# Kernel optimization log

Hardware: AMD Instinct MI355X
Metric: run time of the kernel (lower is better)

## Reference

```python
import jax, jax.numpy as jnp
from jax import lax
import numpy as np

DIM = 768        # d_model (mamba-130m)
D_IN = 1024      # vision encoder feature dim
NQ = 384         # num_queries
NB = 12          # num_blocks
BATCH = 2
LSEQ = 1024      # image tokens
DI = 2 * DIM     # mamba d_inner (expand=2)
DS = 16          # d_state
DC = 4           # d_conv
DTR = 48         # dt_rank = ceil(768/16)
NH = 16          # attention heads
HD = DIM // NH
NM = NB + 2      # mamba instances: fwd-enc, bwd-enc, one per block


def _ln(x, g, b):
    m = jnp.mean(x, -1, keepdims=True)
    v = jnp.mean((x - m) ** 2, -1, keepdims=True)
    return (x - m) * lax.rsqrt(v + 1e-5) * g + b


def _mamba(x, in_w, conv_w, conv_b, xproj_w, dt_w, dt_b, A_log, Dp, out_w):
    # x: (B, L, DIM)
    Bb = x.shape[0]
    xz = x @ in_w.T                      # (B, L, 2*DI)
    xi, z = jnp.split(xz, 2, -1)
    # depthwise causal conv1d over time
    xc = lax.conv_general_dilated(xi.transpose(0, 2, 1), conv_w[:, None, :], (1,),
                                  [(DC - 1, 0)], feature_group_count=DI,
                                  dimension_numbers=('NCH', 'OIH', 'NCH'))
    xc = jax.nn.silu((xc + conv_b[None, :, None]).transpose(0, 2, 1))  # (B, L, DI)
    dbl = xc @ xproj_w.T                 # (B, L, DTR + 2*DS)
    dt, Bm, Cm = jnp.split(dbl, [DTR, DTR + DS], -1)
    dt = jax.nn.softplus(dt @ dt_w.T + dt_b)   # (B, L, DI)
    A = -jnp.exp(A_log)                        # (DI, DS)
    dA = jnp.exp(dt[..., None] * A)            # (B, L, DI, DS)
    dBx = dt[..., None] * Bm[:, :, None, :] * xc[..., None]

    def step(h, inp):
        dA_t, dBx_t, C_t = inp
        h = dA_t * h + dBx_t
        return h, jnp.einsum('bds,bs->bd', h, C_t)

    h0 = jnp.zeros((Bb, DI, DS), x.dtype)
    _, ys = lax.scan(step, h0, (dA.transpose(1, 0, 2, 3), dBx.transpose(1, 0, 2, 3), Cm.transpose(1, 0, 2)))
    y = ys.transpose(1, 0, 2) + Dp * xc
    y = y * jax.nn.silu(z)
    return y @ out_w.T


def _local_allowed(nq, nk):
    # matches Attention.get_local_mask: query i attends to its contiguous key block
    kpq, extra = nk // nq, nk % nq
    i = jnp.arange(nq)
    start = i * kpq + jnp.minimum(i, extra)
    end = start + kpq + (i < extra)
    k = jnp.arange(nk)
    return (k[None, :] >= start[:, None]) & (k[None, :] < end[:, None])


def _mha(q_in, kv, in_w, in_b, out_w, out_b, allowed):
    # nn.MultiheadAttention(dim, 16, batch_first=True) cross-attention
    wq, wk, wv = jnp.split(in_w, 3, 0)
    bq, bk, bv = jnp.split(in_b, 3, 0)
    Bb = q_in.shape[0]
    q = (q_in @ wq.T + bq).reshape(Bb, -1, NH, HD)
    k = (kv @ wk.T + bk).reshape(Bb, -1, NH, HD)
    v = (kv @ wv.T + bv).reshape(Bb, -1, NH, HD)
    s = jnp.einsum('bqhd,bkhd->bhqk', q, k) / np.float32(np.sqrt(HD))
    s = jnp.where(allowed[None, None], s, -jnp.inf)
    a = jax.nn.softmax(s, -1)
    o = jnp.einsum('bhqk,bkhd->bqhd', a, v).reshape(Bb, -1, DIM)
    return o @ out_w.T + out_b


def _model(img_emb, queries, vision_proj_w, vision_proj_b, ln_vision_g, ln_vision_b,
           mamba_in_w, mamba_conv_w, mamba_conv_b, mamba_xproj_w, mamba_dt_w, mamba_dt_b,
           mamba_A_log, mamba_D, mamba_out_w, seq_norm_g, seq_norm_b,
           attn_in_w, attn_in_b, attn_out_w, attn_out_b, cross_w, cross_b):
    mp = lambda i: (mamba_in_w[i], mamba_conv_w[i], mamba_conv_b[i], mamba_xproj_w[i],
                    mamba_dt_w[i], mamba_dt_b[i], mamba_A_log[i], mamba_D[i], mamba_out_w[i])
    feats = _ln(img_emb @ vision_proj_w.T + vision_proj_b, ln_vision_g, ln_vision_b)
    fwd = _mamba(feats, *mp(0))
    bwd = jnp.flip(_mamba(jnp.flip(feats, 1), *mp(1)), 1)
    c = fwd + bwd + feats
    x = jnp.broadcast_to(queries, (img_emb.shape[0], NQ, DIM))
    allowed = _local_allowed(NQ, c.shape[1])
    for l in range(NB):
        x = _ln(x, seq_norm_g[l], seq_norm_b[l])
        x = _mamba(x, *mp(l + 2)) + x
        score = _mha(x, c, attn_in_w[l], attn_in_b[l], attn_out_w[l], attn_out_b[l], allowed)
        x = jnp.concatenate([x, score], -1) @ cross_w[l].T + cross_b[l]
    return x


_model_jit = jax.jit(_model)


def setup_inputs() -> dict:
    key = jax.random.key(0)
    ks = iter(jax.random.split(key, 24))
    rn = lambda shape, s=0.02: jax.random.normal(next(ks), shape, jnp.float32) * s
    A_log = jnp.broadcast_to(jnp.log(jnp.arange(1, DS + 1, dtype=jnp.float32)), (NM, DI, DS))
    return {
        'img_emb': rn((BATCH, LSEQ, D_IN), 1.0),
        'queries': rn((1, NQ, DIM)),
        'vision_proj_w': rn((DIM, D_IN)),
        'vision_proj_b': jnp.zeros((DIM,), jnp.float32),
        'ln_vision_g': jnp.ones((DIM,), jnp.float32),
        'ln_vision_b': jnp.zeros((DIM,), jnp.float32),
        'mamba_in_w': rn((NM, 2 * DI, DIM)),
        'mamba_conv_w': rn((NM, DI, DC), 0.1),
        'mamba_conv_b': jnp.zeros((NM, DI), jnp.float32),
        'mamba_xproj_w': rn((NM, DTR + 2 * DS, DI)),
        'mamba_dt_w': rn((NM, DI, DTR), 0.1),
        'mamba_dt_b': rn((NM, DI), 0.5),
        'mamba_A_log': A_log,
        'mamba_D': jnp.ones((NM, DI), jnp.float32),
        'mamba_out_w': rn((NM, DIM, DI)),
        'seq_norm_g': jnp.ones((NB, DIM), jnp.float32),
        'seq_norm_b': jnp.zeros((NB, DIM), jnp.float32),
        'attn_in_w': rn((NB, 3 * DIM, DIM)),
        'attn_in_b': jnp.zeros((NB, 3 * DIM), jnp.float32),
        'attn_out_w': rn((NB, DIM, DIM)),
        'attn_out_b': jnp.zeros((NB, DIM), jnp.float32),
        'cross_w': rn((NB, DIM, 2 * DIM)),
        'cross_b': jnp.zeros((NB, DIM), jnp.float32),
    }


def reference(img_emb, queries, vision_proj_w, vision_proj_b, ln_vision_g, ln_vision_b,
              mamba_in_w, mamba_conv_w, mamba_conv_b, mamba_xproj_w, mamba_dt_w, mamba_dt_b,
              mamba_A_log, mamba_D, mamba_out_w, seq_norm_g, seq_norm_b,
              attn_in_w, attn_in_b, attn_out_w, attn_out_b, cross_w, cross_b):
    return _model_jit(img_emb, queries, vision_proj_w, vision_proj_b, ln_vision_g, ln_vision_b,
                      mamba_in_w, mamba_conv_w, mamba_conv_b, mamba_xproj_w, mamba_dt_w, mamba_dt_b,
                      mamba_A_log, mamba_D, mamba_out_w, seq_norm_g, seq_norm_b,
                      attn_in_w, attn_in_b, attn_out_w, attn_out_b, cross_w, cross_b)
```

## Files before the change

kernel.cpp:

```cpp
#include <hip/hip_runtime.h>
#include <hip/hip_bf16.h>

#define DIMQ 768
#define D_IN 1024
#define NQ 384
#define NBK 12
#define BATCH 2
#define LSEQ 1024
#define DI 1536
#define DS 16
#define DTR 48
#define NH 16
#define HD 48

typedef __attribute__((ext_vector_type(8))) short short8;
typedef __attribute__((ext_vector_type(4))) float f32x4;

#define GF_BIAS 1
#define GF_SOFTPLUS 2
#define EPI_BIAS 1
#define EPI_ADDT 2

#define LOG2E 1.4426950408889634f

__device__ __forceinline__ unsigned short f2bf(float f) {
    unsigned int u = __builtin_bit_cast(unsigned int, f);
    u = (u + 0x7FFFu + ((u >> 16) & 1u)) >> 16;
    return (unsigned short)u;
}
__device__ __forceinline__ float bf2f(unsigned short h) {
    unsigned int u = ((unsigned int)h) << 16;
    return __builtin_bit_cast(float, u);
}

__device__ __forceinline__ void gload_lds16(const void* g, void* l) {
    __builtin_amdgcn_global_load_lds(
        (const __attribute__((address_space(1))) void*)g,
        (__attribute__((address_space(3))) void*)l, 16, 0, 0);
}

struct WTab {
    const float* src[10];
    long long dstOff[10];
    long long ps[10];
    int cum[10];
    int rows[10], cols[10], dcols[10];
    int n;
    int total;
};

__global__ void wconv_kernel(unsigned short* __restrict__ dst, WTab T)
{
    const int i = blockIdx.x * 256 + threadIdx.x;
    if (i >= T.total) return;
    int sI = 0;
    while (i >= T.cum[sI]) ++sI;
    const int e = i - (sI ? T.cum[sI - 1] : 0);
    const int dcols = T.dcols[sI];
    const int r = e / dcols;
    const int c = e - r * dcols;
    float v = 0.f;
    if (r < T.rows[sI] && c < T.cols[sI]) v = T.src[sI][(long long)r * T.cols[sI] + c];
    const unsigned short h = f2bf(v);
    const unsigned short l = f2bf(v - bf2f(h));
    dst[T.dstOff[sI] + e] = h;
    dst[T.dstOff[sI] + T.ps[sI] + e] = l;
}

struct LTab {
    const float* src[7];
    long long srcStride[7], dstOff[7], ps[7];
    int rows[7], cols[7], dcols[7], cum[7];
};

__global__ __launch_bounds__(256)
void wconv_layers(unsigned short* __restrict__ dst, long long layerStride, int lBase, LTab T)
{
    const int e = blockIdx.x * 256 + threadIdx.x;
    const int l = blockIdx.y + lBase;
    int sI = 0;
    while (e >= T.cum[sI]) ++sI;
    const int eo = e - (sI ? T.cum[sI - 1] : 0);
    const int dc = T.dcols[sI];
    const int r = eo / dc;
    const int c = eo - r * dc;
    float v = 0.f;
    if (r < T.rows[sI] && c < T.cols[sI])
        v = T.src[sI][(long long)l * T.srcStride[sI] + (long long)r * T.cols[sI] + c];
    const unsigned short h = f2bf(v);
    const unsigned short lo2 = f2bf(v - bf2f(h));
    unsigned short* d = dst + (long long)blockIdx.y * layerStride + T.dstOff[sI];
    d[eo] = h;
    d[T.ps[sI] + eo] = lo2;
}

__global__ __launch_bounds__(256, 3)
void gemm_direct(const float* __restrict__ Ag, const unsigned short* __restrict__ Bhl,
                 float* __restrict__ Cg, const float* __restrict__ biasg,
                 int M, int N, int K, int lda, int ldb, int ldc,
                 long long sA, long long sB, long long sC, long long sBias,
                 long long planeB, int flags)
{
    __shared__ __align__(16) unsigned short As[2][2][64][40];
    __shared__ __align__(16) unsigned short Bs[2][2][128][32];

    const int z = blockIdx.z;
    const float* A = Ag + (size_t)z * sA;
    const unsigned short* Bhi = Bhl + (size_t)z * sB;
    const unsigned short* Blo = Bhi + planeB;
    float* C = Cg + (size_t)z * sC;

    const int mBase = blockIdx.x * 64;
    const int nBase = blockIdx.y * 128;
    const int tid = threadIdx.x, lane = tid & 63, wave = tid >> 6;
    const int lm = lane & 15, lq = lane >> 4;
    const int wn = wave * 32;
    const int arow = tid >> 2, aq = tid & 3;
    const int brow = lane >> 2;
    const int bcol = (lane & 3) * 8;

    const int ktiles = (K + 31) >> 5;

    auto issueB = [&](int t, int buf) {
#pragma unroll
        for (int cc = 0; cc < 4; ++cc) {
            const int chunk = wave * 4 + cc;
            const int pl = chunk >> 3;
            const int r16 = chunk & 7;
            const unsigned short* bp = pl ? Blo : Bhi;
            const int n = nBase + r16 * 16 + brow;
            gload_lds16(bp + (size_t)n * ldb + t * 32 + bcol, &Bs[buf][pl][r16 * 16][0]);
        }
    };
    auto loadA = [&](int t, float* v) {
        const int col = t * 32 + aq * 8;
        const float* src = A + (size_t)(mBase + arow) * lda + col;
#pragma unroll
        for (int u = 0; u < 2; ++u) {
            float4 t4 = make_float4(0.f, 0.f, 0.f, 0.f);
            if (col + u * 4 < K) t4 = *(const float4*)(src + u * 4);
            v[u*4+0]=t4.x; v[u*4+1]=t4.y; v[u*4+2]=t4.z; v[u*4+3]=t4.w;
        }
    };
    auto writeA = [&](const float* v, int buf) {
        short8 ph, plv;
#pragma unroll
        for (int j = 0; j < 8; ++j) {
            unsigned short h = f2bf(v[j]);
            ph[j] = (short)h;
            plv[j] = (short)f2bf(v[j] - bf2f(h));
        }
        *(short8*)&As[buf][0][arow][aq * 8] = ph;
        *(short8*)&As[buf][1][arow][aq * 8] = plv;
    };

    float av[8];
    issueB(0, 0);
    loadA(0, av);
    writeA(av, 0);

    f32x4 acc[4][2] = {};
    for (int t = 0; t < ktiles; ++t) {
        const int buf = t & 1;
        __syncthreads();
        const bool more = (t + 1) < ktiles;
        if (more) { issueB(t + 1, buf ^ 1); loadA(t + 1, av); }
        short8 ah[4], al[4], bh[2], bl[2];
#pragma unroll
        for (int i = 0; i < 4; ++i) {
            ah[i] = *(const short8*)&As[buf][0][16*i + lm][lq * 8];
            al[i] = *(const short8*)&As[buf][1][16*i + lm][lq * 8];
        }
#pragma unroll
        for (int j = 0; j < 2; ++j) {
            bh[j] = *(const short8*)&Bs[buf][0][wn + 16*j + lm][lq * 8];
            bl[j] = *(const short8*)&Bs[buf][1][wn + 16*j + lm][lq * 8];
        }
#pragma unroll
        for (int i = 0; i < 4; ++i)
#pragma unroll
            for (int j = 0; j < 2; ++j) {
                acc[i][j] = __builtin_amdgcn_mfma_f32_16x16x32_bf16(ah[i], bh[j], acc[i][j], 0, 0, 0);
                acc[i][j] = __builtin_amdgcn_mfma_f32_16x16x32_bf16(ah[i], bl[j], acc[i][j], 0, 0, 0);
                acc[i][j] = __builtin_amdgcn_mfma_f32_16x16x32_bf16(al[i], bh[j], acc[i][j], 0, 0, 0);
            }
        if (more) writeA(av, buf ^ 1);
    }

#pragma unroll
    for (int i = 0; i < 4; ++i)
#pragma unroll
        for (int j = 0; j < 2; ++j)
#pragma unroll
            for (int r = 0; r < 4; ++r) {
                const int m = mBase + i*16 + lq*4 + r;
                const int n = nBase + wn + j*16 + lm;
                float v = acc[i][j][r];
                if (flags & GF_BIAS)     v += biasg[(size_t)z * sBias + n];
                if (flags & GF_SOFTPLUS) v = (v > 20.f) ? v : log1pf(expf(v));
                C[(size_t)m * ldc + n] = v;
            }
}

__global__ __launch_bounds__(256, 3)
void gemm_splitk(const float* __restrict__ Ag, const unsigned short* __restrict__ Bhl,
                 float* __restrict__ Cp,
                 int M, int kLen, int S, int lda, int ldb, int ldP,
                 long long sA, long long sB, long long planeB)
{
    __shared__ __align__(16) unsigned short As[2][2][64][40];
    __shared__ __align__(16) unsigned short Bs[2][2][128][32];

    const int bz = blockIdx.z;
    const int s = bz % S, z = bz / S;
    const int kOff = s * kLen;
    const float* A = Ag + (size_t)z * sA;
    const unsigned short* Bhi = Bhl + (size_t)z * sB;
    const unsigned short* Blo = Bhi + planeB;

    const int mBase = blockIdx.x * 64;
    const int nBase = blockIdx.y * 128;
    const int tid = threadIdx.x, lane = tid & 63, wave = tid >> 6;
    const int lm = lane & 15, lq = lane >> 4;
    const int wn = wave * 32;
    const int arow = tid >> 2, aq = tid & 3;
    const int brow = lane >> 2;
    const int bcol = (lane & 3) * 8;

    const int ktiles = kLen >> 5;

    auto issueB = [&](int t, int buf) {
#pragma unroll
        for (int cc = 0; cc < 4; ++cc) {
            const int chunk = wave * 4 + cc;
            const int pl = chunk >> 3;
            const int r16 = chunk & 7;
            const unsigned short* bp = pl ? Blo : Bhi;
            const int n = nBase + r16 * 16 + brow;
            gload_lds16(bp + (size_t)n * ldb + kOff + t * 32 + bcol, &Bs[buf][pl][r16 * 16][0]);
        }
    };
    auto loadA = [&](int t, float* v) {
        const float* src = A + (size_t)(mBase + arow) * lda + kOff + t * 32 + aq * 8;
#pragma unroll
        for (int u = 0; u < 2; ++u) {
            const float4 t4 = *(const float4*)(src + u * 4);
            v[u*4+0]=t4.x; v[u*4+1]=t4.y; v[u*4+2]=t4.z; v[u*4+3]=t4.w;
        }
    };
    auto writeA = [&](const float* v, int buf) {
        short8 ph, plv;
#pragma unroll
        for (int j = 0; j < 8; ++j) {
            unsigned short h = f2bf(v[j]);
            ph[j] = (short)h;
            plv[j] = (short)f2bf(v[j] - bf2f(h));
        }
        *(short8*)&As[buf][0][arow][aq * 8] = ph;
        *(short8*)&As[buf][1][arow][aq * 8] = plv;
    };

    float av[8];
    issueB(0, 0);
    loadA(0, av);
    writeA(av, 0);

    f32x4 acc[4][2] = {};
    for (int t = 0; t < ktiles; ++t) {
        const int buf = t & 1;
        __syncthreads();
        const bool more = (t + 1) < ktiles;
        if (more) { issueB(t + 1, buf ^ 1); loadA(t + 1, av); }
        short8 ah[4], al[4], bh[2], bl[2];
#pragma unroll
        for (int i = 0; i < 4; ++i) {
            ah[i] = *(const short8*)&As[buf][0][16*i + lm][lq * 8];
            al[i] = *(const short8*)&As[buf][1][16*i + lm][lq * 8];
        }
#pragma unroll
        for (int j = 0; j < 2; ++j) {
            bh[j] = *(const short8*)&Bs[buf][0][wn + 16*j + lm][lq * 8];
            bl[j] = *(const short8*)&Bs[buf][1][wn + 16*j + lm][lq * 8];
        }
#pragma unroll
        for (int i = 0; i < 4; ++i)
#pragma unroll
            for (int j = 0; j < 2; ++j) {
                acc[i][j] = __builtin_amdgcn_mfma_f32_16x16x32_bf16(ah[i], bh[j], acc[i][j], 0, 0, 0);
                acc[i][j] = __builtin_amdgcn_mfma_f32_16x16x32_bf16(ah[i], bl[j], acc[i][j], 0, 0, 0);
                acc[i][j] = __builtin_amdgcn_mfma_f32_16x16x32_bf16(al[i], bh[j], acc[i][j], 0, 0, 0);
            }
        if (more) writeA(av, buf ^ 1);
    }

    float* Cb = Cp + (size_t)bz * M * ldP;
#pragma unroll
    for (int i = 0; i < 4; ++i)
#pragma unroll
        for (int j = 0; j < 2; ++j)
#pragma unroll
            for (int r = 0; r < 4; ++r) {
                const int m = mBase + i*16 + lq*4 + r;
                const int n = nBase + wn + j*16 + lm;
                Cb[(size_t)m * ldP + n] = acc[i][j][r];
            }
}

__global__ void epi_kernel(const float* __restrict__ Cp, float* __restrict__ outF,
                           const float* __restrict__ bias, const float* __restrict__ addT,
                           int Z, int S, int M, int N, int ldP, int ldOut,
                           long long sOutZ, long long sBiasZ, int ldAdd, int flags)
{
    const int n4 = N >> 2;
    const int idx = blockIdx.x * 256 + threadIdx.x;
    if (idx >= Z * M * n4) return;
    const int c4 = idx % n4;
    const int rem = idx / n4;
    const int m = rem % M;
    const int z = rem / M;
    const int n = c4 * 4;
    const float* base = Cp + ((size_t)z * S * M + m) * ldP + n;
    float4 v = *(const float4*)base;
    for (int s = 1; s < S; ++s) {
        const float4 u = *(const float4*)(base + (size_t)s * M * ldP);
        v.x += u.x; v.y += u.y; v.z += u.z; v.w += u.w;
    }
    if (flags & EPI_BIAS) {
        const float4 b4 = *(const float4*)(bias + (size_t)z * sBiasZ + n);
        v.x += b4.x; v.y += b4.y; v.z += b4.z; v.w += b4.w;
    }
    if (flags & EPI_ADDT) {
        const float4 a4 = *(const float4*)(addT + (size_t)m * ldAdd + n);
        v.x += a4.x; v.y += a4.y; v.z += a4.z; v.w += a4.w;
    }
    *(float4*)(outF + (size_t)z * sOutZ + (size_t)m * ldOut + n) = v;
}

__global__ __launch_bounds__(256)
void epi_ln_kernel(const float* __restrict__ Cp, float* __restrict__ outF,
                   const float* __restrict__ bias,
                   const float* __restrict__ g, const float* __restrict__ b,
                   int S, int M, int ldP)
{
    const int m = blockIdx.x;
    const int tid = threadIdx.x;
    __shared__ float red[8];
    float v[3];
    float s = 0.f, s2 = 0.f;
#pragma unroll
    for (int j = 0; j < 3; ++j) {
        const int n = tid + j * 256;
        const float* pp = Cp + (size_t)m * ldP + n;
        float x = pp[0];
        for (int q = 1; q < S; ++q) x += pp[(size_t)q * M * ldP];
        x += bias[n];
        v[j] = x; s += x; s2 += x * x;
    }
#pragma unroll
    for (int o = 32; o; o >>= 1) { s += __shfl_xor(s, o); s2 += __shfl_xor(s2, o); }
    const int wv = tid >> 6;
    if ((tid & 63) == 0) { red[wv] = s; red[4 + wv] = s2; }
    __syncthreads();
    s  = red[0] + red[1] + red[2] + red[3];
    s2 = red[4] + red[5] + red[6] + red[7];
    const float mean = s * (1.f/768.f);
    const float var  = s2 * (1.f/768.f) - mean * mean;
    const float inv  = rsqrtf(var + 1e-5f);
#pragma unroll
    for (int j = 0; j < 3; ++j) {
        const int n = tid + j * 256;
        outF[(size_t)m * DIMQ + n] = (v[j] - mean) * inv * g[n] + b[n];
    }
}

__global__ void ln_kernel(const float* __restrict__ in, float* __restrict__ out,
                          const float* __restrict__ g, const float* __restrict__ b,
                          int rows, int srcMod)
{
    const int row = blockIdx.x * 4 + (threadIdx.x >> 6);
    const int lane = threadIdx.x & 63;
    if (row >= rows) return;
    const float* p = in + (size_t)(row % srcMod) * DIMQ;
    float v[12], s = 0.f, s2 = 0.f;
#pragma unroll
    for (int j = 0; j < 12; ++j) {
        v[j] = p[j*64 + lane];
        s += v[j];
        s2 += v[j]*v[j];
    }
#pragma unroll
    for (int o = 32; o; o >>= 1) { s += __shfl_xor(s, o); s2 += __shfl_xor(s2, o); }
    const float mean = s * (1.f/768.f);
    const float var  = s2 * (1.f/768.f) - mean*mean;
    const float inv  = rsqrtf(var + 1e-5f);
    float* q = out + (size_t)row * DIMQ;
#pragma unroll
    for (int j = 0; j < 12; ++j) {
        const int c = j*64 + lane;
        q[c] = (v[j] - mean) * inv * g[c] + b[c];
    }
}

__global__ void conv_kernel(const float* __restrict__ xz, float* __restrict__ xc,
                            const float* __restrict__ cw, const float* __restrict__ cb,
                            int Bn, int L, int instShift)
{
    const int idx = blockIdx.x * 256 + threadIdx.x;
    const int total = Bn * L * (DI/4);
    if (idx >= total) return;
    const int d4 = idx % (DI/4);
    const int t  = (idx / (DI/4)) % L;
    const int b  = idx / (L * (DI/4));
    const int inst = b >> instShift;
    const int d = d4 * 4;
    const float* base = xz + (size_t)(b * L) * 3072 + d;
    const float4 w0 = *(const float4*)(cw + (size_t)(inst*DI + d + 0) * 4);
    const float4 w1 = *(const float4*)(cw + (size_t)(inst*DI + d + 1) * 4);
    const float4 w2 = *(const float4*)(cw + (size_t)(inst*DI + d + 2) * 4);
    const float4 w3 = *(const float4*)(cw + (size_t)(inst*DI + d + 3) * 4);
    float4 acc = *(const float4*)(cb + (size_t)inst*DI + d);
    float4 xv[4];
#pragma unroll
    for (int j = 0; j < 4; ++j) {
        const int tt = t - 3 + j;
        xv[j] = (tt >= 0) ? *(const float4*)(base + (size_t)tt * 3072) : make_float4(0,0,0,0);
    }
    acc.x += xv[0].x*w0.x + xv[1].x*w0.y + xv[2].x*w0.z + xv[3].x*w0.w;
    acc.y += xv[0].y*w1.x + xv[1].y*w1.y + xv[2].y*w1.z + xv[3].y*w1.w;
    acc.z += xv[0].z*w2.x + xv[1].z*w2.y + xv[2].z*w2.z + xv[3].z*w2.w;
    acc.w += xv[0].w*w3.x + xv[1].w*w3.y + xv[2].w*w3.z + xv[3].w*w3.w;
    float4 o;
    o.x = acc.x / (1.f + expf(-acc.x));
    o.y = acc.y / (1.f + expf(-acc.y));
    o.z = acc.z / (1.f + expf(-acc.z));
    o.w = acc.w / (1.f + expf(-acc.w));
    *(float4*)(xc + (size_t)(b * L + t) * DI + d) = o;
}

__global__ __launch_bounds__(256)
void scan_p1(const float* __restrict__ dt, const float* __restrict__ dbl,
             const float* __restrict__ xc, const float* __restrict__ A_log,
             float* __restrict__ hend, float* __restrict__ sumdt,
             int L, int CL, int Bn, int instShift)
{
    const int d = blockIdx.x * 256 + threadIdx.x;
    const int b = blockIdx.y;
    const int c = blockIdx.z;
    const int inst = b >> instShift;
    const float* ap = A_log + ((size_t)inst * DI + d) * DS;
    float A2[16];
#pragma unroll
    for (int s = 0; s < 16; ++s) A2[s] = -expf(ap[s]) * LOG2E;
    float h[16] = {};
    float sd = 0.f;
    const int t0 = c * CL;
    const size_t rowbase = (size_t)b * L;
    for (int t = t0; t < t0 + CL; ++t) {
        const size_t row = rowbase + t;
        const float dtv = dt[row * DI + d];
        const float xcv = xc[row * DI + d];
        float Bv[16];
        *(float4*)(Bv + 0)  = *(const float4*)(dbl + row * 80 + 48);
        *(float4*)(Bv + 4)  = *(const float4*)(dbl + row * 80 + 52);
        *(float4*)(Bv + 8)  = *(const float4*)(dbl + row * 80 + 56);
        *(float4*)(Bv + 12) = *(const float4*)(dbl + row * 80 + 60);
        sd += dtv;
        const float bx = dtv * xcv;
#pragma unroll
        for (int s = 0; s < 16; ++s)
            h[s] = exp2f(dtv * A2[s]) * h[s] + bx * Bv[s];
    }
    float* hp = hend + (((size_t)c * Bn + b) * DI + d) * DS;
#pragma unroll
    for (int s = 0; s < 16; s += 4)
        *(float4*)(hp + s) = make_float4(h[s], h[s+1], h[s+2], h[s+3]);
    sumdt[((size_t)c * Bn + b) * DI + d] = sd;
}

__global__ void scan_p2(const float* __restrict__ hend, const float* __restrict__ sumdt,
                        const float* __restrict__ A_log, float* __restrict__ hstart,
                        int NC, int Bn, int instShift)
{
    const int gid = blockIdx.x * 256 + threadIdx.x;
    const int s = gid & 15;
    const int rem = gid >> 4;
    const int d = rem % DI;
    const int b = rem / DI;
    const int inst = b >> instShift;
    const float A2 = -expf(A_log[((size_t)inst * DI + d) * DS + s]) * LOG2E;
    float carry = 0.f;
    for (int c = 0; c < NC; ++c) {
        const size_t off = (((size_t)c * Bn + b) * DI + d) * DS + s;
        hstart[off] = carry;
        carry = exp2f(A2 * sumdt[((size_t)c * Bn + b) * DI + d]) * carry + hend[off];
    }
}

__global__ __launch_bounds__(256)
void scan_p3(const float* __restrict__ dt, const float* __restrict__ dbl,
             const float* __restrict__ xc, const float* __restrict__ xz,
             const float* __restrict__ A_log, const float* __restrict__ Dp,
             const float* __restrict__ hstart, float* __restrict__ y,
             int L, int CL, int Bn, int instShift)
{
    const int d = blockIdx.x * 256 + threadIdx.x;
    const int b = blockIdx.y;
    const int c = blockIdx.z;
    const int inst = b >> instShift;
    const float* ap = A_log + ((size_t)inst * DI + d) * DS;
    float A2[16];
#pragma unroll
    for (int s = 0; s < 16; ++s) A2[s] = -expf(ap[s]) * LOG2E;
    const float Dd = Dp[(size_t)inst * DI + d];
    float h[16];
    const float* hp = hstart + (((size_t)c * Bn + b) * DI + d) * DS;
#pragma unroll
    for (int s = 0; s < 16; s += 4) {
        const float4 t4 = *(const float4*)(hp + s);
        h[s] = t4.x; h[s+1] = t4.y; h[s+2] = t4.z; h[s+3] = t4.w;
    }
    const int t0 = c * CL;
    const size_t rowbase = (size_t)b * L;
    for (int t = t0; t < t0 + CL; ++t) {
        const size_t row = rowbase + t;
        const float dtv = dt[row * DI + d];
        const float xcv = xc[row * DI + d];
        const float zv  = xz[row * 3072 + DI + d];
        float Bv[16], Cv[16];
        *(float4*)(Bv + 0)  = *(const float4*)(dbl + row * 80 + 48);
        *(float4*)(Bv + 4)  = *(const float4*)(dbl + row * 80 + 52);
        *(float4*)(Bv + 8)  = *(const float4*)(dbl + row * 80 + 56);
        *(float4*)(Bv + 12) = *(const float4*)(dbl + row * 80 + 60);
        *(float4*)(Cv + 0)  = *(const float4*)(dbl + row * 80 + 64);
        *(float4*)(Cv + 4)  = *(const float4*)(dbl + row * 80 + 68);
        *(float4*)(Cv + 8)  = *(const float4*)(dbl + row * 80 + 72);
        *(float4*)(Cv + 12) = *(const float4*)(dbl + row * 80 + 76);
        const float bx = dtv * xcv;
#pragma unroll
        for (int s = 0; s < 16; ++s)
            h[s] = exp2f(dtv * A2[s]) * h[s] + bx * Bv[s];
        float p0 = 0.f, p1 = 0.f, p2 = 0.f, p3 = 0.f;
#pragma unroll
        for (int s = 0; s < 4; ++s) {
            p0 += h[s]      * Cv[s];
            p1 += h[s + 4]  * Cv[s + 4];
            p2 += h[s + 8]  * Cv[s + 8];
            p3 += h[s + 12] * Cv[s + 12];
        }
        const float p = (p0 + p1) + (p2 + p3);
        y[row * DI + d] = (p + Dd * xcv) * (zv / (1.f + expf(-zv)));
    }
}

__global__ void attn_kernel(const float* __restrict__ q, const float* __restrict__ kv,
                            float* __restrict__ o)
{
    const int bi = blockIdx.x;
    const int b = bi / NQ, i = bi % NQ;
    const int tid = threadIdx.x;
    const int h = tid >> 2, r = tid & 3;
    int start, len;
    if (i < 256) { start = 3*i; len = 3; } else { start = 2*i + 256; len = 2; }
    const float* qp = q + (size_t)bi * DIMQ + h*48 + r*12;
    float qv[12];
#pragma unroll
    for (int u = 0; u < 12; ++u) qv[u] = qp[u];
    float s[3] = {-1e30f, -1e30f, -1e30f};
    for (int j = 0; j < len; ++j) {
        const float* kp = kv + (size_t)(b*LSEQ + start + j) * 1536 + h*48 + r*12;
        float p = 0.f;
#pragma unroll
        for (int u = 0; u < 12; ++u) p += qv[u] * kp[u];
        p += __shfl_xor(p, 1);
        p += __shfl_xor(p, 2);
        s[j] = p * 0.14433756729740644f;
    }
    const float mx = fmaxf(s[0], fmaxf(s[1], s[2]));
    float e[3];
    e[0] = expf(s[0]-mx); e[1] = expf(s[1]-mx); e[2] = expf(s[2]-mx);
    const float inv = 1.f / (e[0] + e[1] + e[2]);
    float ov[12] = {};
    for (int j = 0; j < len; ++j) {
        const float w = e[j] * inv;
        const float* vp = kv + (size_t)(b*LSEQ + start + j) * 1536 + 768 + h*48 + r*12;
#pragma unroll
        for (int u = 0; u < 12; ++u) ov[u] += w * vp[u];
    }
    float* op = o + (size_t)bi * DIMQ + h*48 + r*12;
#pragma unroll
    for (int u = 0; u < 12; ++u) op[u] = ov[u];
}

__global__ void flip_kernel(float* __restrict__ X2)
{
    const int idx = blockIdx.x * 256 + threadIdx.x;
    if (idx >= 2*1024*192) return;
    const int d4 = idx % 192;
    const int t  = (idx / 192) % 1024;
    const int b  = idx / (192 * 1024);
    const size_t dst = ((size_t)((2+b)*1024 + t)) * DIMQ + d4*4;
    const size_t src = ((size_t)(b*1024 + (1023 - t))) * DIMQ + d4*4;
    *(float4*)(X2 + dst) = *(const float4*)(X2 + src);
}

__global__ void combine_kernel(const float* __restrict__ oe, const float* __restrict__ feats,
                               float* __restrict__ c)
{
    const int idx = blockIdx.x * 256 + threadIdx.x;
    if (idx >= 2*1024*192) return;
    const int d4 = idx % 192;
    const int t  = (idx / 192) % 1024;
    const int b  = idx / (192 * 1024);
    const size_t fw = ((size_t)(b*1024 + t)) * DIMQ + d4*4;
    const size_t bw = ((size_t)((2+b)*1024 + (1023 - t))) * DIMQ + d4*4;
    const float4 a = *(const float4*)(oe + fw);
    const float4 bb = *(const float4*)(oe + bw);
    const float4 f = *(const float4*)(feats + fw);
    float4 o;
    o.x = a.x + bb.x + f.x; o.y = a.y + bb.y + f.y;
    o.z = a.z + bb.z + f.z; o.w = a.w + bb.w + f.w;
    *(float4*)(c + fw) = o;
}

extern "C" void kernel_launch(void* const* d_in, const int* in_sizes, int n_in,
                              void* d_out, int out_size, void* d_ws, size_t ws_size,
                              hipStream_t stream) {
    const float* img_emb  = (const float*)d_in[0];
    const float* queries  = (const float*)d_in[1];
    const float* vis_w    = (const float*)d_in[2];
    const float* vis_b    = (const float*)d_in[3];
    const float* lnv_g    = (const float*)d_in[4];
    const float* lnv_b    = (const float*)d_in[5];
    const float* m_in_w   = (const float*)d_in[6];
    const float* m_conv_w = (const float*)d_in[7];
    const float* m_conv_b = (const float*)d_in[8];
    const float* m_xp_w   = (const float*)d_in[9];
    const float* m_dt_w   = (const float*)d_in[10];
    const float* m_dt_b   = (const float*)d_in[11];
    const float* m_A_log  = (const float*)d_in[12];
    const float* m_D      = (const float*)d_in[13];
    const float* m_out_w  = (const float*)d_in[14];
    const float* sn_g     = (const float*)d_in[15];
    const float* sn_b     = (const float*)d_in[16];
    const float* a_in_w   = (const float*)d_in[17];
    const float* a_in_b   = (const float*)d_in[18];
    const float* a_out_w  = (const float*)d_in[19];
    const float* a_out_b  = (const float*)d_in[20];
    const float* cr_w     = (const float*)d_in[21];
    const float* cr_b     = (const float*)d_in[22];
    float* out = (float*)d_out;

    float* ws = (float*)d_ws;
    auto alloc = [&](size_t n) { float* p = ws; ws += n; return p; };
    float* X2   = alloc((size_t)4096*768);
    float* xzb  = alloc((size_t)4096*3072);
    float* xcb  = alloc((size_t)4096*1536);
    float* dblb = alloc((size_t)4096*80);
    float* dtb  = alloc((size_t)4096*1536);
    float* yb   = alloc((size_t)4096*1536);
    float* oe   = alloc((size_t)4096*768);
    float* cbuf = alloc((size_t)2048*768);
    float* xn   = alloc((size_t)768*768);
    float* x1s  = alloc((size_t)768*1536);
    float* qb   = alloc((size_t)768*768);
    float* ob   = alloc((size_t)768*768);
    float* Cp   = alloc((size_t)2359296);
    unsigned short* wenc = (unsigned short*)alloc((size_t)16908288/2);

    const long long LAYER_USH = 14745600;
    const size_t usedFloats = (size_t)(ws - (float*)d_ws);
    const size_t needFull = (usedFloats + (size_t)12 * (LAYER_USH/2)) * 4;
    const bool bigW = ws_size >= needFull;
    unsigned short* wlayAll = (unsigned short*)ws;

    const size_t kvFloats = (size_t)12 * 2048 * 1536;
    const size_t needKV = needFull + kvFloats * 4;
    const bool kvHoist = bigW && ws_size >= needKV;
    float* kvAll = (float*)(wlayAll + (size_t)12 * LAYER_USH);

    const long long P_VIS = 768LL*1024;
    const long long P_IN  = 3072LL*768;
    const long long P_XP  = 128LL*1536;
    const long long P_DT  = 1536LL*64;
    const long long P_OUT = 768LL*1536;
    const long long P_AIN = 2304LL*768;
    const long long P_AOUT= 768LL*768;
    const long long P_CR  = 768LL*1536;
    const long long off_vis   = 0;
    const long long off_encIn = 2*P_VIS;
    const long long off_encXp = off_encIn + 4*P_IN;
    const long long off_encDt = off_encXp + 4*P_XP;
    const long long off_encOut= off_encDt + 4*P_DT;
    const long long off_in  = 0;
    const long long off_xp  = 2*P_IN;
    const long long off_dt  = off_xp + 2*P_XP;
    const long long off_out = off_dt + 2*P_DT;
    const long long off_aIn = off_out + 2*P_OUT;
    const long long off_aOut= off_aIn + 2*P_AIN;
    const long long off_cr  = off_aOut + 2*P_AOUT;

    auto addSeg = [](WTab& T, const float* src, int rows, int cols, int drows, int dcols,
                     long long dstOff) {
        const int k = T.n;
        T.src[k] = src; T.rows[k] = rows; T.cols[k] = cols; T.dcols[k] = dcols;
        T.ps[k] = (long long)drows * dcols;
        T.dstOff[k] = dstOff;
        T.total += drows * dcols;
        T.cum[k] = T.total;
        T.n = k + 1;
    };

    auto GD = [&](const float* A, const unsigned short* Bhl, long long planeB,
                  float* C, const float* bias,
                  int M, int N, int K, int lda, int ldb, int ldc,
                  long long sA, long long sB, long long sC, long long sBias,
                  int Z, int flags) {
        dim3 grid(M/64, N/128, Z);
        gemm_direct<<<grid, 256, 0, stream>>>(A, Bhl, C, bias, M, N, K, lda, ldb, ldc,
                                              sA, sB, sC, sBias, planeB, flags);
    };
    auto GS = [&](const float* A, const unsigned short* Bhl, long long planeB,
                  int M, int Ntile, int kLen, int S, int lda, int ldb, int ldP,
                  long long sA, long long sB, int Z) {
        dim3 grid(M/64, Ntile/128, Z*S);
        gemm_splitk<<<grid, 256, 0, stream>>>(A, Bhl, Cp, M, kLen, S, lda, ldb, ldP,
                                              sA, sB, planeB);
    };
    auto EPI = [&](float* outF, const float* bias, const float* addT,
                   int Z, int S, int M, int N, int ldP, int ldOut,
                   long long sOutZ, long long sBiasZ, int ldAdd, int flags) {
        const int total = Z * M * (N/4);
        epi_kernel<<<(total+255)/256, 256, 0, stream>>>(Cp, outF, bias, addT, Z, S, M, N,
                                                        ldP, ldOut, sOutZ, sBiasZ, ldAdd, flags);
    };

    {
        WTab T = {}; T.n = 0; T.total = 0;
        addSeg(T, vis_w, 768, 1024, 768, 1024, off_vis);
        addSeg(T, m_in_w,               3072, 768, 3072, 768, off_encIn);
        addSeg(T, m_in_w + 3072*768,    3072, 768, 3072, 768, off_encIn + 2*P_IN);
        addSeg(T, m_xp_w,               80, 1536, 128, 1536, off_encXp);
        addSeg(T, m_xp_w + 80*1536,     80, 1536, 128, 1536, off_encXp + 2*P_XP);
        addSeg(T, m_dt_w,               1536, 48, 1536, 64, off_encDt);
        addSeg(T, m_dt_w + 1536*48,     1536, 48, 1536, 64, off_encDt + 2*P_DT);
        addSeg(T, m_out_w,              768, 1536, 768, 1536, off_encOut);
        addSeg(T, m_out_w + 768*1536,   768, 1536, 768, 1536, off_encOut + 2*P_OUT);
        wconv_kernel<<<(T.total+255)/256, 256, 0, stream>>>(wenc, T);
    }

    LTab LT = {};
    {
        auto seg = [&](int k, const float* src, long long srcStride, int rows, int cols,
                       int drows, int dcols, long long dstOff) {
            LT.src[k] = src; LT.srcStride[k] = srcStride;
            LT.rows[k] = rows; LT.cols[k] = cols; LT.dcols[k] = dcols;
            LT.ps[k] = (long long)drows * dcols; LT.dstOff[k] = dstOff;
            LT.cum[k] = (k ? LT.cum[k-1] : 0) + drows * dcols;
        };
        seg(0, m_in_w  + (size_t)2*3072*768, 3072LL*768, 3072, 768, 3072, 768, off_in);
        seg(1, m_xp_w  + (size_t)2*80*1536,  80LL*1536,  80, 1536, 128, 1536, off_xp);
        seg(2, m_dt_w  + (size_t)2*1536*48,  1536LL*48,  1536, 48, 1536, 64, off_dt);
        seg(3, m_out_w + (size_t)2*768*1536, 768LL*1536, 768, 1536, 768, 1536, off_out);
        seg(4, a_in_w,  2304LL*768, 2304, 768, 2304, 768, off_aIn);
        seg(5, a_out_w, 768LL*768,  768, 768, 768, 768, off_aOut);
        seg(6, cr_w,    768LL*1536, 768, 1536, 768, 1536, off_cr);
    }
    if (bigW)
        wconv_layers<<<dim3(28800, 12), 256, 0, stream>>>(wlayAll, LAYER_USH, 0, LT);

    GD(img_emb, wenc + off_vis, P_VIS, oe, vis_b,
       2048, 768, 1024, 1024, 1024, 768, 0,0,0,0, 1, GF_BIAS);
    ln_kernel<<<512, 256, 0, stream>>>(oe, X2, lnv_g, lnv_b, 2048, 2048);
    flip_kernel<<<(2*1024*192 + 255)/256, 256, 0, stream>>>(X2);

    GD(X2, wenc + off_encIn, P_IN, xzb, nullptr,
       2048, 3072, 768, 768, 768, 3072, 2048LL*768, 2*P_IN, 2048LL*3072, 0, 2, 0);
    conv_kernel<<<(4*1024*384 + 255)/256, 256, 0, stream>>>(xzb, xcb, m_conv_w, m_conv_b, 4, 1024, 1);
    GS(xcb, wenc + off_encXp, P_XP, 2048, 128, 384, 4, 1536, 1536, 128,
       2048LL*1536, 2*P_XP, 2);
    EPI(dblb, nullptr, nullptr, 2, 4, 2048, 80, 128, 80, 2048LL*80, 0, 0, 0);
    GD(dblb, wenc + off_encDt, P_DT, dtb, m_dt_b,
       2048, 1536, 48, 80, 64, 1536, 2048LL*80, 2*P_DT, 2048LL*1536, 1536, 2,
       GF_BIAS | GF_SOFTPLUS);
    {
        const int NC = 16, CL = 64;
        float* hend   = oe;
        float* hstart = oe + (size_t)NC*4*DI*DS;
        float* sumdt  = cbuf;
        scan_p1<<<dim3(6, 4, NC), 256, 0, stream>>>(dtb, dblb, xcb, m_A_log, hend, sumdt, 1024, CL, 4, 1);
        scan_p2<<<(4*DI*DS)/256, 256, 0, stream>>>(hend, sumdt, m_A_log, hstart, NC, 4, 1);
        scan_p3<<<dim3(6, 4, NC), 256, 0, stream>>>(dtb, dblb, xcb, xzb, m_A_log, m_D, hstart, yb, 1024, CL, 4, 1);
    }
    GD(yb, wenc + off_encOut, P_OUT, oe, nullptr,
       2048, 768, 1536, 1536, 1536, 768, 2048LL*1536, 2*P_OUT, 2048LL*768, 0, 2, 0);
    combine_kernel<<<(2*1024*192 + 255)/256, 256, 0, stream>>>(oe, X2, cbuf);

    if (kvHoist)
        GD(cbuf, wlayAll + off_aIn + 768LL*768, P_AIN, kvAll, a_in_b + 768,
           2048, 1536, 768, 768, 768, 1536,
           0, LAYER_USH, 2048LL*1536, 2304, 12, GF_BIAS);

    ln_kernel<<<192, 256, 0, stream>>>(queries, xn, sn_g, sn_b, 768, 384);

    for (int l = 0; l < NBK; ++l) {
        const int li = l + 2;
        const unsigned short* wl = bigW ? wlayAll + (size_t)l * LAYER_USH : wlayAll;
        if (!bigW)
            wconv_layers<<<dim3(28800, 1), 256, 0, stream>>>((unsigned short*)wlayAll, LAYER_USH, l, LT);

        GD(xn, wl + off_in, P_IN, xzb, nullptr,
           768, 3072, 768, 768, 768, 3072, 0,0,0,0, 1, 0);
        conv_kernel<<<(2*NQ*384 + 255)/256, 256, 0, stream>>>(
            xzb, xcb, m_conv_w + (size_t)li*DI*4, m_conv_b + (size_t)li*DI, 2, NQ, 8);
        GS(xcb, wl + off_xp, P_XP, 768, 128, 96, 16, 1536, 1536, 128, 0, 0, 1);
        EPI(dblb, nullptr, nullptr, 1, 16, 768, 80, 128, 80, 0, 0, 0, 0);
        GD(dblb, wl + off_dt, P_DT, dtb, m_dt_b + (size_t)li*1536,
           768, 1536, 48, 80, 64, 1536, 0,0,0,0, 1, GF_BIAS | GF_SOFTPLUS);
        {
            const int NC = 24, CL = 16;
            const float* Ap = m_A_log + (size_t)li*DI*DS;
            float* hend   = oe;
            float* hstart = oe + (size_t)NC*2*DI*DS;
            float* sumdt  = oe + (size_t)2*NC*2*DI*DS;
            scan_p1<<<dim3(6, 2, NC), 256, 0, stream>>>(dtb, dblb, xcb, Ap, hend, sumdt, NQ, CL, 2, 8);
            scan_p2<<<(2*DI*DS)/256, 256, 0, stream>>>(hend, sumdt, Ap, hstart, NC, 2, 8);
            scan_p3<<<dim3(6, 2, NC), 256, 0, stream>>>(dtb, dblb, xcb, xzb, Ap, m_D + (size_t)li*DI,
                                                        hstart, yb, NQ, CL, 2, 8);
        }
        GS(yb, wl + off_out, P_OUT, 768, 768, 384, 4, 1536, 1536, 768, 0, 0, 1);
        EPI(x1s, nullptr, xn, 1, 4, 768, 768, 768, 1536, 0, 0, 768, EPI_ADDT);
        GS(x1s, wl + off_aIn, P_AIN, 768, 768, 192, 4, 1536, 768, 768, 0, 0, 1);
        EPI(qb, a_in_b + (size_t)l*2304, nullptr, 1, 4, 768, 768, 768, 768, 0, 0, 0, EPI_BIAS);
        const float* kvp;
        if (kvHoist) {
            kvp = kvAll + (size_t)l * 2048 * 1536;
        } else {
            GD(cbuf, wl + off_aIn + 768LL*768, P_AIN, oe, a_in_b + (size_t)l*2304 + 768,
               2048, 1536, 768, 768, 768, 1536, 0,0,0,0, 1, GF_BIAS);
            kvp = oe;
        }
        attn_kernel<<<2*NQ, 64, 0, stream>>>(qb, kvp, ob);
        GS(ob, wl + off_aOut, P_AOUT, 768, 768, 192, 4, 768, 768, 768, 0, 0, 1);
        EPI(x1s + 768, a_out_b + (size_t)l*768, nullptr, 1, 4, 768, 768, 768, 1536, 0, 0, 0, EPI_BIAS);
        GS(x1s, wl + off_cr, P_CR, 768, 768, 384, 4, 1536, 1536, 768, 0, 0, 1);
        if (l == NBK - 1) {
            EPI(out, cr_b + (size_t)l*768, nullptr, 1, 4, 768, 768, 768, 768, 0, 0, 0, EPI_BIAS);
        } else {
            epi_ln_kernel<<<768, 256, 0, stream>>>(Cp, xn, cr_b + (size_t)l*768,
                                                   sn_g + (size_t)(l+1)*768,
                                                   sn_b + (size_t)(l+1)*768,
                                                   4, 768, 768);
        }
    }
}
```

Baseline: 4.160 ms.

## Fuse chunk-carry scan into final scan pass and fold q split-K reduce into attention

Removes the separate scan_p2 carry-propagation kernel: each scan_p3f block now recomputes its starting state by iterating over all previous chunks' end states and summed dt. It also drops the EPI reduction for the query projection, so the attention kernel sums the split-K partials from Cp and adds the bias itself. This saves two launches per layer plus the hstart and qb round trips, at the cost of redundant prefix work in later chunks (up to 23 chunks of 16-wide state per thread) and strided partial reads inside attention.

```diff
diff --git a/kernel.cpp b/kernel.cpp
--- a/kernel.cpp
+++ b/kernel.cpp
@@ -477,31 +477,13 @@
     sumdt[((size_t)c * Bn + b) * DI + d] = sd;
 }
 
-__global__ void scan_p2(const float* __restrict__ hend, const float* __restrict__ sumdt,
-                        const float* __restrict__ A_log, float* __restrict__ hstart,
-                        int NC, int Bn, int instShift)
-{
-    const int gid = blockIdx.x * 256 + threadIdx.x;
-    const int s = gid & 15;
-    const int rem = gid >> 4;
-    const int d = rem % DI;
-    const int b = rem / DI;
-    const int inst = b >> instShift;
-    const float A2 = -expf(A_log[((size_t)inst * DI + d) * DS + s]) * LOG2E;
-    float carry = 0.f;
-    for (int c = 0; c < NC; ++c) {
-        const size_t off = (((size_t)c * Bn + b) * DI + d) * DS + s;
-        hstart[off] = carry;
-        carry = exp2f(A2 * sumdt[((size_t)c * Bn + b) * DI + d]) * carry + hend[off];
-    }
-}
-
 __global__ __launch_bounds__(256)
-void scan_p3(const float* __restrict__ dt, const float* __restrict__ dbl,
-             const float* __restrict__ xc, const float* __restrict__ xz,
-             const float* __restrict__ A_log, const float* __restrict__ Dp,
-             const float* __restrict__ hstart, float* __restrict__ y,
-             int L, int CL, int Bn, int instShift)
+void scan_p3f(const float* __restrict__ dt, const float* __restrict__ dbl,
+              const float* __restrict__ xc, const float* __restrict__ xz,
+              const float* __restrict__ A_log, const float* __restrict__ Dp,
+              const float* __restrict__ hend, const float* __restrict__ sumdt,
+              float* __restrict__ y,
+              int L, int CL, int Bn, int instShift)
 {
     const int d = blockIdx.x * 256 + threadIdx.x;
     const int b = blockIdx.y;
@@ -512,13 +494,22 @@
 #pragma unroll
     for (int s = 0; s < 16; ++s) A2[s] = -expf(ap[s]) * LOG2E;
     const float Dd = Dp[(size_t)inst * DI + d];
-    float h[16];
-    const float* hp = hstart + (((size_t)c * Bn + b) * DI + d) * DS;
-#pragma unroll
-    for (int s = 0; s < 16; s += 4) {
-        const float4 t4 = *(const float4*)(hp + s);
-        h[s] = t4.x; h[s+1] = t4.y; h[s+2] = t4.z; h[s+3] = t4.w;
-    }
+
+    float h[16] = {};
+    for (int cp = 0; cp < c; ++cp) {
+        const float sd = sumdt[((size_t)cp * Bn + b) * DI + d];
+        const float* hp = hend + (((size_t)cp * Bn + b) * DI + d) * DS;
+        float he[16];
+#pragma unroll
+        for (int s = 0; s < 16; s += 4) {
+            const float4 t4 = *(const float4*)(hp + s);
+            he[s] = t4.x; he[s+1] = t4.y; he[s+2] = t4.z; he[s+3] = t4.w;
+        }
+#pragma unroll
+        for (int s = 0; s < 16; ++s)
+            h[s] = exp2f(A2[s] * sd) * h[s] + he[s];
+    }
+
     const int t0 = c * CL;
     const size_t rowbase = (size_t)b * L;
     for (int t = t0; t < t0 + CL; ++t) {
@@ -552,8 +543,9 @@
     }
 }
 
-__global__ void attn_kernel(const float* __restrict__ q, const float* __restrict__ kv,
-                            float* __restrict__ o)
+__global__ void attn_kernel(const float* __restrict__ qP, const float* __restrict__ qBias,
+                            const float* __restrict__ kv, float* __restrict__ o,
+                            int S, int ldP)
 {
     const int bi = blockIdx.x;
     const int b = bi / NQ, i = bi % NQ;
@@ -561,13 +553,18 @@
     const int h = tid >> 2, r = tid & 3;
     int start, len;
     if (i < 256) { start = 3*i; len = 3; } else { start = 2*i + 256; len = 2; }
-    const float* qp = q + (size_t)bi * DIMQ + h*48 + r*12;
+    const int col0 = h*48 + r*12;
     float qv[12];
 #pragma unroll
-    for (int u = 0; u < 12; ++u) qv[u] = qp[u];
+    for (int u = 0; u < 12; ++u) {
+        const int n = col0 + u;
+        float x = qP[(size_t)bi * ldP + n];
+        for (int s = 1; s < S; ++s) x += qP[((size_t)s * 768 + bi) * ldP + n];
+        qv[u] = x + qBias[n];
+    }
     float s[3] = {-1e30f, -1e30f, -1e30f};
     for (int j = 0; j < len; ++j) {
-        const float* kp = kv + (size_t)(b*LSEQ + start + j) * 1536 + h*48 + r*12;
+        const float* kp = kv + (size_t)(b*LSEQ + start + j) * 1536 + col0;
         float p = 0.f;
 #pragma unroll
         for (int u = 0; u < 12; ++u) p += qv[u] * kp[u];
@@ -582,11 +579,11 @@
     float ov[12] = {};
     for (int j = 0; j < len; ++j) {
         const float w = e[j] * inv;
-        const float* vp = kv + (size_t)(b*LSEQ + start + j) * 1536 + 768 + h*48 + r*12;
+        const float* vp = kv + (size_t)(b*LSEQ + start + j) * 1536 + 768 + col0;
 #pragma unroll
         for (int u = 0; u < 12; ++u) ov[u] += w * vp[u];
     }
-    float* op = o + (size_t)bi * DIMQ + h*48 + r*12;
+    float* op = o + (size_t)bi * DIMQ + col0;
 #pragma unroll
     for (int u = 0; u < 12; ++u) op[u] = ov[u];
 }
@@ -662,7 +659,6 @@
     float* cbuf = alloc((size_t)2048*768);
     float* xn   = alloc((size_t)768*768);
     float* x1s  = alloc((size_t)768*1536);
-    float* qb   = alloc((size_t)768*768);
     float* ob   = alloc((size_t)768*768);
     float* Cp   = alloc((size_t)2359296);
     unsigned short* wenc = (unsigned short*)alloc((size_t)16908288/2);
@@ -785,11 +781,10 @@
     {
         const int NC = 16, CL = 64;
         float* hend   = oe;
-        float* hstart = oe + (size_t)NC*4*DI*DS;
-        float* sumdt  = cbuf;
+        float* sumdt  = oe + (size_t)NC*4*DI*DS;
         scan_p1<<<dim3(6, 4, NC), 256, 0, stream>>>(dtb, dblb, xcb, m_A_log, hend, sumdt, 1024, CL, 4, 1);
-        scan_p2<<<(4*DI*DS)/256, 256, 0, stream>>>(hend, sumdt, m_A_log, hstart, NC, 4, 1);
-        scan_p3<<<dim3(6, 4, NC), 256, 0, stream>>>(dtb, dblb, xcb, xzb, m_A_log, m_D, hstart, yb, 1024, CL, 4, 1);
+        scan_p3f<<<dim3(6, 4, NC), 256, 0, stream>>>(dtb, dblb, xcb, xzb, m_A_log, m_D,
+                                                     hend, sumdt, yb, 1024, CL, 4, 1);
     }
     GD(yb, wenc + off_encOut, P_OUT, oe, nullptr,
        2048, 768, 1536, 1536, 1536, 768, 2048LL*1536, 2*P_OUT, 2048LL*768, 0, 2, 0);
@@ -820,17 +815,14 @@
             const int NC = 24, CL = 16;
             const float* Ap = m_A_log + (size_t)li*DI*DS;
             float* hend   = oe;
-            float* hstart = oe + (size_t)NC*2*DI*DS;
-            float* sumdt  = oe + (size_t)2*NC*2*DI*DS;
+            float* sumdt  = oe + (size_t)NC*2*DI*DS;
             scan_p1<<<dim3(6, 2, NC), 256, 0, stream>>>(dtb, dblb, xcb, Ap, hend, sumdt, NQ, CL, 2, 8);
-            scan_p2<<<(2*DI*DS)/256, 256, 0, stream>>>(hend, sumdt, Ap, hstart, NC, 2, 8);
-            scan_p3<<<dim3(6, 2, NC), 256, 0, stream>>>(dtb, dblb, xcb, xzb, Ap, m_D + (size_t)li*DI,
-                                                        hstart, yb, NQ, CL, 2, 8);
+            scan_p3f<<<dim3(6, 2, NC), 256, 0, stream>>>(dtb, dblb, xcb, xzb, Ap, m_D + (size_t)li*DI,
+                                                         hend, sumdt, yb, NQ, CL, 2, 8);
         }
         GS(yb, wl + off_out, P_OUT, 768, 768, 384, 4, 1536, 1536, 768, 0, 0, 1);
         EPI(x1s, nullptr, xn, 1, 4, 768, 768, 768, 1536, 0, 0, 768, EPI_ADDT);
         GS(x1s, wl + off_aIn, P_AIN, 768, 768, 192, 4, 1536, 768, 768, 0, 0, 1);
-        EPI(qb, a_in_b + (size_t)l*2304, nullptr, 1, 4, 768, 768, 768, 768, 0, 0, 0, EPI_BIAS);
         const float* kvp;
         if (kvHoist) {
             kvp = kvAll + (size_t)l * 2048 * 1536;
@@ -839,7 +831,7 @@
                2048, 1536, 768, 768, 768, 1536, 0,0,0,0, 1, GF_BIAS);
             kvp = oe;
         }
-        attn_kernel<<<2*NQ, 64, 0, stream>>>(qb, kvp, ob);
+        attn_kernel<<<2*NQ, 64, 0, stream>>>(Cp, a_in_b + (size_t)l*2304, kvp, ob, 4, 768);
         GS(ob, wl + off_aOut, P_AOUT, 768, 768, 192, 4, 768, 768, 768, 0, 0, 1);
         EPI(x1s + 768, a_out_b + (size_t)l*768, nullptr, 1, 4, 768, 768, 768, 1536, 0, 0, 0, EPI_BIAS);
         GS(x1s, wl + off_cr, P_CR, 768, 768, 384, 4, 1536, 1536, 768, 0, 0, 1);
```

After: 4.285 ms. 1.03x slower.
